# Kernel optimization log

Measured on AMD Instinct MI355X. Metric: run time of the kernel, lower is better.

## Reference

```python
import jax, jax.numpy as jnp
from jax import lax
import numpy as np

INPUT_SIZE, HIDDEN, NUM_LAYERS, OUTPUT = 64, 512, 2, 1024
BATCH, SEQ = 64, 1024


def setup_inputs() -> dict:
    key = jax.random.key(0)
    ks = jax.random.split(key, 11)
    s = 1.0 / np.sqrt(HIDDEN)
    u = lambda k, shape: jax.random.uniform(k, shape, jnp.float32, -s, s)
    return {
        "x": jax.random.normal(ks[0], (BATCH, SEQ, INPUT_SIZE), jnp.float32),
        # layer 0 (PyTorch gate order: i, f, g, o stacked along dim 0)
        "W_ih0": u(ks[1], (4 * HIDDEN, INPUT_SIZE)),
        "W_hh0": u(ks[2], (4 * HIDDEN, HIDDEN)),
        "b_ih0": u(ks[3], (4 * HIDDEN,)),
        "b_hh0": u(ks[4], (4 * HIDDEN,)),
        # layer 1
        "W_ih1": u(ks[5], (4 * HIDDEN, HIDDEN)),
        "W_hh1": u(ks[6], (4 * HIDDEN, HIDDEN)),
        "b_ih1": u(ks[7], (4 * HIDDEN,)),
        "b_hh1": u(ks[8], (4 * HIDDEN,)),
        # fc
        "fc_w": u(ks[9], (OUTPUT, HIDDEN)),
        "fc_b": u(ks[10], (OUTPUT,)),
    }


def _lstm_layer(x, W_ih, W_hh, b_ih, b_hh):
    # x: [B, T, D]. Precompute input projection for all timesteps (one big GEMM).
    B = x.shape[0]
    H = W_hh.shape[1]
    xw = jnp.einsum('btd,gd->btg', x, W_ih) + b_ih + b_hh  # [B, T, 4H]
    xw = jnp.swapaxes(xw, 0, 1)  # [T, B, 4H] for scan
    h0 = jnp.zeros((B, H), x.dtype)
    c0 = jnp.zeros((B, H), x.dtype)

    def step(carry, xw_t):
        h, c = carry
        gates = xw_t + h @ W_hh.T  # [B, 4H]
        i, f, g, o = jnp.split(gates, 4, axis=-1)
        c = jax.nn.sigmoid(f) * c + jax.nn.sigmoid(i) * jnp.tanh(g)
        h = jax.nn.sigmoid(o) * jnp.tanh(c)
        return (h, c), h

    (h_T, c_T), hs = lax.scan(step, (h0, c0), xw)
    return jnp.swapaxes(hs, 0, 1), h_T  # [B, T, H], [B, H]


def _forward(x, W_ih0, W_hh0, b_ih0, b_hh0, W_ih1, W_hh1, b_ih1, b_hh1, fc_w, fc_b):
    ula0, h0_T = _lstm_layer(x, W_ih0, W_hh0, b_ih0, b_hh0)
    ula1, h1_T = _lstm_layer(ula0, W_ih1, W_hh1, b_ih1, b_hh1)
    # h_out: [num_layers, B, H] -> view(-1, H)
    h_out = jnp.concatenate([h0_T, h1_T], axis=0)  # [L*B, H]
    out = h_out @ fc_w.T + fc_b
    out = jax.nn.relu(out)
    # Dropout(p=0.2): identity in eval mode (deterministic reference)
    return out


def reference(x, W_ih0, W_hh0, b_ih0, b_hh0, W_ih1, W_hh1, b_ih1, b_hh1, fc_w, fc_b):
    return _forward(x, W_ih0, W_hh0, b_ih0, b_hh0, W_ih1, W_hh1, b_ih1, b_hh1, fc_w, fc_b)
```

## Files before the change

kernel.cpp:

```cpp
#include <hip/hip_runtime.h>


#define H      512
#define T_SEQ  1024
#define DIN    64
#define STEPS  1025

#define SLOT_U32 16384
#define GRP_U32  49152
#define WS_BYTES (4 * GRP_U32 * 4)

typedef _Float16 f16x8 __attribute__((ext_vector_type(8)));
typedef float    f32x4 __attribute__((ext_vector_type(4)));
typedef unsigned long long u64t;

__device__ __forceinline__ u64t ld_u64(const u64t* p) {
  return __hip_atomic_load((u64t*)p, __ATOMIC_RELAXED, __HIP_MEMORY_SCOPE_AGENT);
}
__device__ __forceinline__ void st_u64(u64t* p, u64t v) {
  __hip_atomic_store(p, v, __ATOMIC_RELAXED, __HIP_MEMORY_SCOPE_AGENT);
}
__device__ __forceinline__ f16x8 pk8(float4 a, float4 b) {
  f16x8 r;
  r[0] = (_Float16)a.x; r[1] = (_Float16)a.y; r[2] = (_Float16)a.z; r[3] = (_Float16)a.w;
  r[4] = (_Float16)b.x; r[5] = (_Float16)b.y; r[6] = (_Float16)b.z; r[7] = (_Float16)b.w;
  return r;
}
__device__ __forceinline__ f16x8 cvt8(const float* p) {
  return pk8(*(const float4*)p, *(const float4*)(p + 4));
}
__device__ __forceinline__ f32x4 mfma16(f16x8 a, f16x8 b, f32x4 c) {
  return __builtin_amdgcn_mfma_f32_16x16x32_f16(a, b, c, 0, 0, 0);
}
__device__ __forceinline__ float rcpf_(float x) {
#if __has_builtin(__builtin_amdgcn_rcpf)
  return __builtin_amdgcn_rcpf(x);
#else
  return 1.0f / x;
#endif
}
__device__ __forceinline__ float sigm(float x) {
  x = fminf(fmaxf(x, -30.f), 30.f);
  return rcpf_(1.f + __expf(-x));
}
__device__ __forceinline__ float tanhx(float x) {
  x = fminf(fmaxf(x, -15.f), 15.f);
  float e = __expf(2.f * x);
  return (e - 1.f) * rcpf_(e + 1.f);
}
__device__ __forceinline__ unsigned payload(u64t v) {
  return ((unsigned)v & 0xffffu) | ((unsigned)(v >> 32) << 16);
}

__global__ __launch_bounds__(256, 1)
void lstm_fused(const float* __restrict__ x,
                const float* __restrict__ Wih0, const float* __restrict__ Whh0,
                const float* __restrict__ bih0, const float* __restrict__ bhh0,
                const float* __restrict__ Wih1, const float* __restrict__ Whh1,
                const float* __restrict__ bih1, const float* __restrict__ bhh1,
                const float* __restrict__ fcw,  const float* __restrict__ fcb,
                float* __restrict__ out, unsigned* __restrict__ ws)
{
  __shared__ unsigned sH[2][8320];

  const int tid  = threadIdx.x;
  const int wid  = blockIdx.x;
  const int g    = wid >> 5;
  const int w    = wid & 31;
  const int wv   = tid >> 6;
  const int lane = tid & 63;
  const int bcol = lane & 15;
  const int kgrp = lane >> 4;
  const int layer = wv >> 1;
  const int hb    = w * 16 + (wv & 1) * 8;

  unsigned* gbase = ws + g * GRP_U32;

  const int src_m = lane & 15;
  const int gr0 = (src_m & 3) * H + hb + 2 * (src_m >> 2);
  const int gr1 = gr0 + 1;
  f16x8 wA[2][32];
  if (layer == 0) {
    #pragma unroll
    for (int f = 0; f < 18; ++f) {
      const float *p0, *p1;
      if (f < 2) {
        p0 = Wih0 + (size_t)gr0 * DIN + f * 32 + kgrp * 8;
        p1 = Wih0 + (size_t)gr1 * DIN + f * 32 + kgrp * 8;
      } else {
        p0 = Whh0 + (size_t)gr0 * H + (f - 2) * 32 + kgrp * 8;
        p1 = Whh0 + (size_t)gr1 * H + (f - 2) * 32 + kgrp * 8;
      }
      wA[0][f] = cvt8(p0); wA[1][f] = cvt8(p1);
    }
  } else {
    #pragma unroll
    for (int f = 0; f < 16; ++f) {
      int col = f * 32 + kgrp * 8;
      wA[0][f] = cvt8(Wih1 + (size_t)gr0 * H + col);
      wA[1][f] = cvt8(Wih1 + (size_t)gr1 * H + col);
    }
    #pragma unroll
    for (int f = 16; f < 32; ++f) {
      int col = (f - 16) * 32 + kgrp * 8;
      wA[0][f] = cvt8(Whh1 + (size_t)gr0 * H + col);
      wA[1][f] = cvt8(Whh1 + (size_t)gr1 * H + col);
    }
  }
  float bias[2][4];
  {
    const float* bi = layer ? bih1 : bih0;
    const float* bh = layer ? bhh1 : bhh0;
    const int u0 = hb + 2 * kgrp, u1 = u0 + 1;
    #pragma unroll
    for (int rr = 0; rr < 4; ++rr) {
      bias[0][rr] = bi[rr * H + u0] + bh[rr * H + u0];
      bias[1][rr] = bi[rr * H + u1] + bh[rr * H + u1];
    }
  }

  for (int i = tid; i < 2 * 8320; i += 256) ((unsigned*)sH)[i] = 0;
  __syncthreads();

  float cst0 = 0.f, cst1 = 0.f;
  unsigned spins = 0;
  const int rowb = bcol * 1040 + kgrp * 16;

  for (int s = 0; s < STEPS; ++s) {
    float4 xr0 = {0,0,0,0}, xr1 = xr0, xr2 = xr0, xr3 = xr0;
    if (layer == 0) {
      int t = (s < T_SEQ) ? s : (T_SEQ - 1);
      const float* xp = x + ((size_t)((g * 16 + bcol) * T_SEQ + t)) * DIN + kgrp * 8;
      xr0 = *(const float4*)xp;        xr1 = *(const float4*)(xp + 4);
      xr2 = *(const float4*)(xp + 32); xr3 = *(const float4*)(xp + 36);
    }
    if (s > 0) {
      const u64t* src = (const u64t*)(gbase + ((s - 1) % 3) * SLOT_U32);
      const unsigned want = (unsigned)s;
      unsigned* dstbuf = sH[s & 1];
      u64t v0[16], v1[16];
      #pragma unroll
      for (int i = 0; i < 16; ++i) v0[i] = ld_u64(src + tid + i * 256);
      for (;;) {
        unsigned bad = 0;
        #pragma unroll
        for (int i = 0; i < 16; ++i) {
          unsigned lo = (unsigned)v0[i], hi = (unsigned)(v0[i] >> 32);
          if (((lo >> 16) ^ want) | ((hi >> 16) ^ want)) bad |= (1u << i);
        }
        if (!bad) break;
        if (++spins > 8000000u) break;
        #pragma unroll
        for (int i = 0; i < 16; ++i)
          if (bad & (1u << i)) v0[i] = ld_u64(src + tid + i * 256);
      }
      #pragma unroll
      for (int i = 0; i < 16; ++i)
        v1[i] = ld_u64(src + tid + (16 + i) * 256);
      #pragma unroll
      for (int i = 0; i < 16; ++i) {
        int j = tid + i * 256;
        dstbuf[(j >> 12) * 4160 + ((j >> 8) & 15) * 260 + (j & 255)] = payload(v0[i]);
      }
      for (;;) {
        unsigned bad = 0;
        #pragma unroll
        for (int i = 0; i < 16; ++i) {
          unsigned lo = (unsigned)v1[i], hi = (unsigned)(v1[i] >> 32);
          if (((lo >> 16) ^ want) | ((hi >> 16) ^ want)) bad |= (1u << i);
        }
        if (!bad) break;
        if (++spins > 8000000u) break;
        #pragma unroll
        for (int i = 0; i < 16; ++i)
          if (bad & (1u << i)) v1[i] = ld_u64(src + tid + (16 + i) * 256);
      }
      #pragma unroll
      for (int i = 0; i < 16; ++i) {
        int j = tid + (16 + i) * 256;
        dstbuf[(j >> 12) * 4160 + ((j >> 8) & 15) * 260 + (j & 255)] = payload(v1[i]);
      }
    }
    __syncthreads();

    const bool act = layer ? (s > 0) : (s < T_SEQ);
    float hv0 = 0.f, hv1 = 0.f;
    if (act) {
      f32x4 a0e = {0,0,0,0}, a0o = {0,0,0,0};
      f32x4 a1e = {0,0,0,0}, a1o = {0,0,0,0};
      const char* cur = (const char*)sH[s & 1];
      if (layer == 0) {
        f16x8 b0 = pk8(xr0, xr1);
        a0e = mfma16(wA[0][0], b0, a0e); a1e = mfma16(wA[1][0], b0, a1e);
        f16x8 b1 = pk8(xr2, xr3);
        a0o = mfma16(wA[0][1], b1, a0o); a1o = mfma16(wA[1][1], b1, a1o);
        #pragma unroll
        for (int f = 2; f < 18; ++f) {
          f16x8 bf = *(const f16x8*)(cur + rowb + (f - 2) * 64);
          if (f & 1) { a0o = mfma16(wA[0][f], bf, a0o); a1o = mfma16(wA[1][f], bf, a1o); }
          else       { a0e = mfma16(wA[0][f], bf, a0e); a1e = mfma16(wA[1][f], bf, a1e); }
        }
      } else {
        #pragma unroll
        for (int f = 0; f < 16; ++f) {
          f16x8 bf = *(const f16x8*)(cur + rowb + f * 64);
          if (f & 1) { a0o = mfma16(wA[0][f], bf, a0o); a1o = mfma16(wA[1][f], bf, a1o); }
          else       { a0e = mfma16(wA[0][f], bf, a0e); a1e = mfma16(wA[1][f], bf, a1e); }
        }
        #pragma unroll
        for (int f = 16; f < 32; ++f) {
          f16x8 bf = *(const f16x8*)(cur + 16640 + rowb + (f - 16) * 64);
          if (f & 1) { a0o = mfma16(wA[0][f], bf, a0o); a1o = mfma16(wA[1][f], bf, a1o); }
          else       { a0e = mfma16(wA[0][f], bf, a0e); a1e = mfma16(wA[1][f], bf, a1e); }
        }
      }
      f32x4 acc0 = a0e + a0o;
      f32x4 acc1 = a1e + a1o;
      {
        float ii = sigm(acc0[0] + bias[0][0]);
        float ff = sigm(acc0[1] + bias[0][1]);
        float gg = tanhx(acc0[2] + bias[0][2]);
        float oo = sigm(acc0[3] + bias[0][3]);
        cst0 = ff * cst0 + ii * gg;
        hv0 = oo * tanhx(cst0);
      }
      {
        float ii = sigm(acc1[0] + bias[1][0]);
        float ff = sigm(acc1[1] + bias[1][1]);
        float gg = tanhx(acc1[2] + bias[1][2]);
        float oo = sigm(acc1[3] + bias[1][3]);
        cst1 = ff * cst1 + ii * gg;
        hv1 = oo * tanhx(cst1);
      }
    }
    const bool produce = layer ? true : (s < T_SEQ);
    if (produce) {
      u64t tag2 = ((u64t)(unsigned)(s + 1) << 16) | ((u64t)(unsigned)(s + 1) << 48);
      u64t e = (u64t)(unsigned)__builtin_bit_cast(unsigned short, (_Float16)hv0);
      u64t o = (u64t)(unsigned)__builtin_bit_cast(unsigned short, (_Float16)hv1);
      u64t* dst = (u64t*)(gbase + (s % 3) * SLOT_U32 + layer * 8192
                          + bcol * 512 + hb) + kgrp;
      st_u64(dst, e | (o << 32) | tag2);
    }
  }

  __syncthreads();

  {
    const int rt = wid >> 4, ct = wid & 15;
    const int sg = rt & 3;
    const bool isH1 = (rt >= 4);
    const unsigned want = isH1 ? (unsigned)STEPS : (unsigned)(STEPS - 1);
    const int     slot  = isH1 ? 1 : 0;
    const u64t* src = (const u64t*)(ws + sg * GRP_U32 + slot * SLOT_U32
                                    + (isH1 ? 8192 : 0));
    u64t v[16];
    #pragma unroll
    for (int i = 0; i < 16; ++i) v[i] = ld_u64(src + tid + i * 256);
    for (;;) {
      unsigned bad = 0;
      #pragma unroll
      for (int i = 0; i < 16; ++i) {
        unsigned lo = (unsigned)v[i], hi = (unsigned)(v[i] >> 32);
        if (((lo >> 16) ^ want) | ((hi >> 16) ^ want)) bad |= (1u << i);
      }
      if (!bad) break;
      if (++spins > 8000000u) break;
      #pragma unroll
      for (int i = 0; i < 16; ++i)
        if (bad & (1u << i)) v[i] = ld_u64(src + tid + i * 256);
    }
    #pragma unroll
    for (int i = 0; i < 16; ++i) {
      int j = tid + i * 256;
      sH[0][(j >> 8) * 260 + (j & 255)] = payload(v[i]);
    }
    __syncthreads();
    const int col = ct * 64 + wv * 16 + bcol;
    f32x4 a0 = {0,0,0,0}, a1 = {0,0,0,0};
    #pragma unroll
    for (int f = 0; f < 16; ++f) {
      f16x8 af = *(const f16x8*)((const char*)sH[0] + rowb + f * 64);
      f16x8 bf = cvt8(fcw + (size_t)col * H + f * 32 + kgrp * 8);
      if (f & 1) a1 = mfma16(af, bf, a1); else a0 = mfma16(af, bf, a0);
    }
    f32x4 a = a0 + a1;
    const float fb = fcb[col];
    #pragma unroll
    for (int rr = 0; rr < 4; ++rr) {
      int row = rt * 16 + kgrp * 4 + rr;
      float v2 = a[rr] + fb;
      out[(size_t)row * 1024 + col] = v2 > 0.f ? v2 : 0.f;
    }
  }
}

extern "C" void kernel_launch(void* const* d_in, const int* in_sizes, int n_in,
                              void* d_out, int out_size, void* d_ws, size_t ws_size,
                              hipStream_t stream) {
  const float* x    = (const float*)d_in[0];
  const float* Wih0 = (const float*)d_in[1];
  const float* Whh0 = (const float*)d_in[2];
  const float* bih0 = (const float*)d_in[3];
  const float* bhh0 = (const float*)d_in[4];
  const float* Wih1 = (const float*)d_in[5];
  const float* Whh1 = (const float*)d_in[6];
  const float* bih1 = (const float*)d_in[7];
  const float* bhh1 = (const float*)d_in[8];
  const float* fcw  = (const float*)d_in[9];
  const float* fcb  = (const float*)d_in[10];
  (void)in_sizes; (void)n_in; (void)out_size; (void)ws_size;

  hipMemsetAsync(d_ws, 0, WS_BYTES, stream);
  lstm_fused<<<dim3(128), dim3(256), 0, stream>>>(
      x, Wih0, Whh0, bih0, bhh0, Wih1, Whh1, bih1, bhh1, fcw, fcb,
      (float*)d_out, (unsigned*)d_ws);
}
```

Measured before the change: 4.022 ms.

## Load layer-1 hidden state directly into registers, stage only layer-0 via LDS

The block previously spun on and staged both layers' hidden states from the global exchange slot into shared memory before any wave could compute. Now only the layer-0 half is staged through LDS, while layer-1 waves prefetch their own h1 fragments straight into 64 registers at the start of the step and poll those for the step tag. They convert the fragments to f16 MFMA operands and do the recurrent half first. This halves the LDS staging and the block-wide wait, and lets layer-1 h arrival overlap with the shared staging. The cost is much higher register pressure (64 u64 values per thread) and per-wave spin loops with redundant global reads.

```diff
diff --git a/kernel.cpp b/kernel.cpp
--- a/kernel.cpp
+++ b/kernel.cpp
@@ -12,6 +12,7 @@
 
 typedef _Float16 f16x8 __attribute__((ext_vector_type(8)));
 typedef float    f32x4 __attribute__((ext_vector_type(4)));
+typedef unsigned u32x4 __attribute__((ext_vector_type(4)));
 typedef unsigned long long u64t;
 
 __device__ __forceinline__ u64t ld_u64(const u64t* p) {
@@ -61,7 +62,7 @@
                 const float* __restrict__ fcw,  const float* __restrict__ fcb,
                 float* __restrict__ out, unsigned* __restrict__ ws)
 {
-  __shared__ unsigned sH[2][8320];
+  __shared__ unsigned sH[2][4160];
 
   const int tid  = threadIdx.x;
   const int wid  = blockIdx.x;
@@ -119,14 +120,23 @@
     }
   }
 
-  for (int i = tid; i < 2 * 8320; i += 256) ((unsigned*)sH)[i] = 0;
+  for (int i = tid; i < 2 * 4160; i += 256) ((unsigned*)sH)[i] = 0;
   __syncthreads();
 
   float cst0 = 0.f, cst1 = 0.f;
   unsigned spins = 0;
   const int rowb = bcol * 1040 + kgrp * 16;
+  const int h1base = bcol * 256 + kgrp * 4;
 
   for (int s = 0; s < STEPS; ++s) {
+    const u64t* slot = (const u64t*)(gbase + ((s > 0 ? s - 1 : 0) % 3) * SLOT_U32);
+    u64t hr[64];
+    if (layer == 1 && s > 0) {
+      const u64t* s1 = slot + 4096;
+      #pragma unroll
+      for (int e = 0; e < 64; ++e)
+        hr[e] = ld_u64(s1 + h1base + (e >> 2) * 16 + (e & 3));
+    }
     float4 xr0 = {0,0,0,0}, xr1 = xr0, xr2 = xr0, xr3 = xr0;
     if (layer == 0) {
       int t = (s < T_SEQ) ? s : (T_SEQ - 1);
@@ -135,12 +145,11 @@
       xr2 = *(const float4*)(xp + 32); xr3 = *(const float4*)(xp + 36);
     }
     if (s > 0) {
-      const u64t* src = (const u64t*)(gbase + ((s - 1) % 3) * SLOT_U32);
       const unsigned want = (unsigned)s;
       unsigned* dstbuf = sH[s & 1];
-      u64t v0[16], v1[16];
-      #pragma unroll
-      for (int i = 0; i < 16; ++i) v0[i] = ld_u64(src + tid + i * 256);
+      u64t v0[16];
+      #pragma unroll
+      for (int i = 0; i < 16; ++i) v0[i] = ld_u64(slot + tid + i * 256);
       for (;;) {
         unsigned bad = 0;
         #pragma unroll
@@ -152,33 +161,12 @@
         if (++spins > 8000000u) break;
         #pragma unroll
         for (int i = 0; i < 16; ++i)
-          if (bad & (1u << i)) v0[i] = ld_u64(src + tid + i * 256);
-      }
-      #pragma unroll
-      for (int i = 0; i < 16; ++i)
-        v1[i] = ld_u64(src + tid + (16 + i) * 256);
+          if (bad & (1u << i)) v0[i] = ld_u64(slot + tid + i * 256);
+      }
       #pragma unroll
       for (int i = 0; i < 16; ++i) {
         int j = tid + i * 256;
-        dstbuf[(j >> 12) * 4160 + ((j >> 8) & 15) * 260 + (j & 255)] = payload(v0[i]);
-      }
-      for (;;) {
-        unsigned bad = 0;
-        #pragma unroll
-        for (int i = 0; i < 16; ++i) {
-          unsigned lo = (unsigned)v1[i], hi = (unsigned)(v1[i] >> 32);
-          if (((lo >> 16) ^ want) | ((hi >> 16) ^ want)) bad |= (1u << i);
-        }
-        if (!bad) break;
-        if (++spins > 8000000u) break;
-        #pragma unroll
-        for (int i = 0; i < 16; ++i)
-          if (bad & (1u << i)) v1[i] = ld_u64(src + tid + (16 + i) * 256);
-      }
-      #pragma unroll
-      for (int i = 0; i < 16; ++i) {
-        int j = tid + (16 + i) * 256;
-        dstbuf[(j >> 12) * 4160 + ((j >> 8) & 15) * 260 + (j & 255)] = payload(v1[i]);
+        dstbuf[(j >> 8) * 260 + (j & 255)] = payload(v0[i]);
       }
     }
     __syncthreads();
@@ -201,15 +189,37 @@
           else       { a0e = mfma16(wA[0][f], bf, a0e); a1e = mfma16(wA[1][f], bf, a1e); }
         }
       } else {
+        const u64t* s1 = slot + 4096;
+        const u64t want64 = ((u64t)(unsigned)s << 48) | ((u64t)(unsigned)s << 16);
+        for (;;) {
+          u64t bad = 0;
+          #pragma unroll
+          for (int e = 0; e < 64; ++e)
+            if ((hr[e] ^ want64) & 0xFFFF0000FFFF0000ull) bad |= (1ull << e);
+          if (!bad) break;
+          if (++spins > 8000000u) break;
+          #pragma unroll
+          for (int e = 0; e < 64; ++e)
+            if (bad & (1ull << e))
+              hr[e] = ld_u64(s1 + h1base + (e >> 2) * 16 + (e & 3));
+        }
+        f16x8 hb1[16];
+        #pragma unroll
+        for (int f = 0; f < 16; ++f) {
+          u32x4 t;
+          t[0] = payload(hr[f * 4 + 0]); t[1] = payload(hr[f * 4 + 1]);
+          t[2] = payload(hr[f * 4 + 2]); t[3] = payload(hr[f * 4 + 3]);
+          hb1[f] = __builtin_bit_cast(f16x8, t);
+        }
+        #pragma unroll
+        for (int f = 0; f < 16; ++f) {
+          f16x8 bf = hb1[f];
+          if (f & 1) { a0o = mfma16(wA[0][16 + f], bf, a0o); a1o = mfma16(wA[1][16 + f], bf, a1o); }
+          else       { a0e = mfma16(wA[0][16 + f], bf, a0e); a1e = mfma16(wA[1][16 + f], bf, a1e); }
+        }
         #pragma unroll
         for (int f = 0; f < 16; ++f) {
           f16x8 bf = *(const f16x8*)(cur + rowb + f * 64);
-          if (f & 1) { a0o = mfma16(wA[0][f], bf, a0o); a1o = mfma16(wA[1][f], bf, a1o); }
-          else       { a0e = mfma16(wA[0][f], bf, a0e); a1e = mfma16(wA[1][f], bf, a1e); }
-        }
-        #pragma unroll
-        for (int f = 16; f < 32; ++f) {
-          f16x8 bf = *(const f16x8*)(cur + 16640 + rowb + (f - 16) * 64);
           if (f & 1) { a0o = mfma16(wA[0][f], bf, a0o); a1o = mfma16(wA[1][f], bf, a1o); }
           else       { a0e = mfma16(wA[0][f], bf, a0e); a1e = mfma16(wA[1][f], bf, a1e); }
         }
```

Result: slower. 10.82 ms (+169.1%).
